# Performance work log

Hardware: AMD Instinct MI355X
Metric: run time of the kernel (lower is better)

Reference implementation:

```python
import jax, jax.numpy as jnp
import numpy as np

B, T, C, H = 128, 256, 64, 128  # batch, seq_len, num_channels, hidden_size


def setup_inputs() -> dict:
    key = jax.random.key(0)
    ks = jax.random.split(key, 7)
    s = 1.0 / np.sqrt(H)  # PyTorch LSTM/Linear init bound
    x = jax.random.normal(ks[0], (B, T, C), dtype=jnp.float32)
    # Per-channel LSTM weights (input_size=1). Gate order i,f,g,o like PyTorch.
    w_ih = jax.random.uniform(ks[1], (C, 4 * H), jnp.float32, -s, s)      # [C,4H] (input is scalar)
    w_hh = jax.random.uniform(ks[2], (C, 4 * H, H), jnp.float32, -s, s)   # [C,4H,H]
    b_ih = jax.random.uniform(ks[3], (C, 4 * H), jnp.float32, -s, s)
    b_hh = jax.random.uniform(ks[4], (C, 4 * H), jnp.float32, -s, s)
    # Per-channel Linear(H, 1) head.
    w_fc = jax.random.uniform(ks[5], (C, H), jnp.float32, -s, s)
    b_fc = jax.random.uniform(ks[6], (C,), jnp.float32, -s, s)
    return {"x": x, "w_ih": w_ih, "w_hh": w_hh, "b_ih": b_ih,
            "b_hh": b_hh, "w_fc": w_fc, "b_fc": b_fc}


def reference(x, w_ih, w_hh, b_ih, b_hh, w_fc, b_fc):
    # x: [B,T,C]. All C channel-LSTMs run as one batched recurrence over [B,C].
    b = b_ih + b_hh  # [C,4H]
    xt = jnp.transpose(x, (1, 0, 2))  # [T,B,C] for scan over time
    h0 = jnp.zeros((x.shape[0], x.shape[2], w_hh.shape[-1]), x.dtype)  # [B,C,H]
    c0 = h0

    def step(carry, x_t):
        h, c = carry  # [B,C,H]
        # scalar input times per-channel input weights + recurrent GEMM
        gates = x_t[..., None] * w_ih + jnp.einsum('bch,cgh->bcg', h, w_hh) + b  # [B,C,4H]
        i, f, g, o = jnp.split(gates, 4, axis=-1)
        i = jax.nn.sigmoid(i)
        f = jax.nn.sigmoid(f)
        g = jnp.tanh(g)
        o = jax.nn.sigmoid(o)
        c_new = f * c + i * g
        h_new = o * jnp.tanh(c_new)
        return (h_new, c_new), None

    (hT, _), _ = jax.lax.scan(step, (h0, c0), xt)
    # Per-channel linear head on the last hidden state -> [B,C]
    return jnp.einsum('bch,ch->bc', hT, w_fc) + b_fc
```

## Files before the change

kernel.cpp:

```cpp
#include <hip/hip_runtime.h>
#include <hip/hip_bf16.h>

typedef __bf16 bf16_t;
typedef bf16_t bf16x8 __attribute__((ext_vector_type(8)));
typedef float f32x4 __attribute__((ext_vector_type(4)));
typedef float f32x2 __attribute__((ext_vector_type(2)));

#define B_   128
#define T_   256
#define C_   64
#define H_   128
#define G_   512
#define BT   16
#define HBUF 2048

#define K1 1.4426950408889634f
#define K2 2.8853900817779268f

union AF { bf16x8 v; uint32_t w[4]; };

__device__ __forceinline__ uint32_t cvt_pk_bf16(float a, float b) {
    uint32_t r; asm("v_cvt_pk_bf16_f32 %0, %1, %2" : "=v"(r) : "v"(a), "v"(b)); return r;
}
__device__ __forceinline__ f32x2 exp2v(f32x2 z) {
    f32x2 r; r.x = __builtin_amdgcn_exp2f(z.x); r.y = __builtin_amdgcn_exp2f(z.y); return r;
}
__device__ __forceinline__ f32x2 rcpv(f32x2 z) {
    f32x2 r; r.x = __builtin_amdgcn_rcpf(z.x); r.y = __builtin_amdgcn_rcpf(z.y); return r;
}

__global__ __launch_bounds__(512, 4) void lstm_fused(
    const float* __restrict__ x,
    const float* __restrict__ w_ih,
    const float* __restrict__ w_hh,
    const float* __restrict__ b_ih,
    const float* __restrict__ b_hh,
    const float* __restrict__ w_fc,
    const float* __restrict__ b_fc,
    float* __restrict__ out)
{
    const int c    = blockIdx.x & (C_ - 1);
    const int bt   = blockIdx.x >> 6;
    const int b0   = bt * BT;
    const int tid  = threadIdx.x;
    const int w    = tid >> 6;
    const int lane = tid & 63;
    const int l16  = lane & 15;
    const int lg   = lane >> 4;
    const bool lg0 = (lg == 0);

    __shared__ __align__(16) bf16_t h_lds[2 * HBUF];
    __shared__ __align__(16) float x_lds[T_ * BT];

    for (int i = tid; i < HBUF; i += 512) ((uint32_t*)h_lds)[i] = 0u;
    for (int i = tid; i < BT * T_; i += 512) {
        const int bl = i >> 8, t = i & 255;
        x_lds[t * BT + bl] = x[(size_t)(b0 + bl) * (T_ * C_) + (size_t)t * C_ + c];
    }

    bf16x8 bw[4][4];
    AF     augb[4];
    #pragma unroll
    for (int q = 0; q < 4; ++q) {
        const float s = (q == 2) ? K2 : -K1;
        const int n = q * 128 + w * 16 + l16;
        #pragma unroll
        for (int kk = 0; kk < 4; ++kk) {
            const int k0 = kk * 32 + lg * 8;
            const float4 wa = *(const float4*)&w_hh[((size_t)(c * G_ + n)) * H_ + k0];
            const float4 wb = *(const float4*)&w_hh[((size_t)(c * G_ + n)) * H_ + k0 + 4];
            bf16x8 g;
            g[0] = (bf16_t)(s * wa.x); g[1] = (bf16_t)(s * wa.y);
            g[2] = (bf16_t)(s * wa.z); g[3] = (bf16_t)(s * wa.w);
            g[4] = (bf16_t)(s * wb.x); g[5] = (bf16_t)(s * wb.y);
            g[6] = (bf16_t)(s * wb.z); g[7] = (bf16_t)(s * wb.w);
            bw[q][kk] = g;
        }
        const float wv = s * w_ih[c * G_ + n];
        const bf16_t wh = (bf16_t)wv;
        const bf16_t wl = (bf16_t)(wv - (float)wh);
        const float bb = s * (b_ih[c * G_ + n] + b_hh[c * G_ + n]);
        const bf16_t bh = (bf16_t)bb;
        const bf16_t bl2 = (bf16_t)(bb - (float)bh);
        bf16x8 f;
        #pragma unroll
        for (int e = 0; e < 8; ++e) f[e] = (bf16_t)0.0f;
        if (lg0) { f[0] = wh; f[1] = wl; f[2] = wh; f[3] = bh; f[4] = bl2; }
        augb[q].v = f;
    }

    float cst[4] = {0.f, 0.f, 0.f, 0.f};
    const f32x4 zc = {0.f, 0.f, 0.f, 0.f};
    const f32x2 one2 = {1.f, 1.f};

    __syncthreads();

    const int a_off = l16 * 8;
    const int wbase = (w * 2 + (l16 >> 3)) * 128 + lg * 32 + (l16 & 7);

    auto step = [&](const int RD, const int WR, const int t) {
        const float xr = x_lds[t * BT + l16];
        const uint32_t p0 = cvt_pk_bf16(xr, xr);
        const float xhf = __uint_as_float(p0 << 16);
        const uint32_t p1 = cvt_pk_bf16(xr - xhf, 1.0f);
        AF a4;
        a4.w[0] = lg0 ? p0 : 0u;
        a4.w[1] = lg0 ? p1 : 0u;
        a4.w[2] = lg0 ? 0x00003F80u : 0u;
        a4.w[3] = 0u;

        f32x4 acc[4];
        {
            #pragma unroll
            for (int q = 0; q < 4; ++q)
                acc[q] = __builtin_amdgcn_mfma_f32_16x16x32_bf16(a4.v, augb[q].v, zc, 0, 0, 0);
        }
        #pragma unroll
        for (int kk = 0; kk < 4; ++kk) {
            const bf16x8 a = *(const bf16x8*)&h_lds[RD + (kk * 4 + lg) * 128 + a_off];
            #pragma unroll
            for (int q = 0; q < 4; ++q)
                acc[q] = __builtin_amdgcn_mfma_f32_16x16x32_bf16(a, bw[q][kk], acc[q], 0, 0, 0);
        }

        #pragma unroll
        for (int p = 0; p < 2; ++p) {
            f32x2 zi = {acc[0][2*p], acc[0][2*p+1]};
            f32x2 zf = {acc[1][2*p], acc[1][2*p+1]};
            f32x2 zg = {acc[2][2*p], acc[2][2*p+1]};
            f32x2 zo = {acc[3][2*p], acc[3][2*p+1]};
            const f32x2 ei = exp2v(zi), ef = exp2v(zf), eg = exp2v(zg), eo = exp2v(zo);
            const f32x2 A2 = one2 + ei, D2 = one2 + ef, B2 = one2 + eg, O2 = one2 + eo;
            const f32x2 AB = A2 * B2;
            const f32x2 r1 = rcpv(D2 * AB);
            f32x2 cs = {cst[2*p], cst[2*p+1]};
            const f32x2 cn = (D2 * (eg - one2) + cs * AB) * r1;
            cst[2*p] = cn.x; cst[2*p+1] = cn.y;
            f32x2 m2 = K2 * cn;
            m2 = __builtin_elementwise_min(__builtin_elementwise_max(m2, f32x2{-60.f,-60.f}), f32x2{60.f,60.f});
            const f32x2 ec = exp2v(m2);
            const f32x2 r2 = rcpv(O2 * (one2 + ec));
            const f32x2 hv = (ec - one2) * r2;
            h_lds[WR + wbase + (2*p)   * 8] = (bf16_t)hv.x;
            h_lds[WR + wbase + (2*p+1) * 8] = (bf16_t)hv.y;
        }
        __syncthreads();
    };

    for (int t = 0; t < T_; t += 2) {
        step(0, HBUF, t);
        step(HBUF, 0, t + 1);
    }

    #pragma unroll
    for (int rr = 0; rr < 2; ++rr) {
        const int row = w * 2 + rr;
        const int eaddr = (lane >> 2) * 128 + row * 8 + (lane & 3) * 2;
        const float h0 = (float)h_lds[eaddr];
        const float h1 = (float)h_lds[eaddr + 1];
        const float2 wf = *(const float2*)&w_fc[c * H_ + 2 * lane];
        float p = h0 * wf.x + h1 * wf.y;
        #pragma unroll
        for (int off = 32; off; off >>= 1) p += __shfl_xor(p, off);
        if (lane == 0) out[(size_t)(b0 + row) * C_ + c] = p + b_fc[c];
    }
}

extern "C" void kernel_launch(void* const* d_in, const int* in_sizes, int n_in,
                              void* d_out, int out_size, void* d_ws, size_t ws_size,
                              hipStream_t stream) {
    const float* x    = (const float*)d_in[0];
    const float* w_ih = (const float*)d_in[1];
    const float* w_hh = (const float*)d_in[2];
    const float* b_ih = (const float*)d_in[3];
    const float* b_hh = (const float*)d_in[4];
    const float* w_fc = (const float*)d_in[5];
    const float* b_fc = (const float*)d_in[6];
    float* out = (float*)d_out;

    dim3 grid(C_ * (B_ / BT));
    dim3 block(512);
    lstm_fused<<<grid, block, 0, stream>>>(x, w_ih, w_hh, b_ih, b_hh, w_fc, b_fc, out);
}
```

Baseline: 347.5 us.

## Interleave two channels per block to overlap MFMA with gate activations

Each block now processes two channels, and the loop staggers them so one channel's recurrent MFMAs run while the other channel's gate activations are computed. The aim is to hide the serial latency of the MFMA→activation→sync chain. The input and bias term moves from an augmented MFMA to fp32 FMAs. Reciprocals are shared between pairs and the tanh clamp uses fmed3. The grid halves, occupancy bounds drop to 2 blocks per CU, and per-thread register pressure doubles, so fewer blocks fill the GPU.

```diff
diff --git a/kernel.cpp b/kernel.cpp
--- a/kernel.cpp
+++ b/kernel.cpp
@@ -12,24 +12,19 @@
 #define H_   128
 #define G_   512
 #define BT   16
-#define HBUF 2048
 
 #define K1 1.4426950408889634f
 #define K2 2.8853900817779268f
 
-union AF { bf16x8 v; uint32_t w[4]; };
-
-__device__ __forceinline__ uint32_t cvt_pk_bf16(float a, float b) {
-    uint32_t r; asm("v_cvt_pk_bf16_f32 %0, %1, %2" : "=v"(r) : "v"(a), "v"(b)); return r;
-}
 __device__ __forceinline__ f32x2 exp2v(f32x2 z) {
     f32x2 r; r.x = __builtin_amdgcn_exp2f(z.x); r.y = __builtin_amdgcn_exp2f(z.y); return r;
 }
-__device__ __forceinline__ f32x2 rcpv(f32x2 z) {
-    f32x2 r; r.x = __builtin_amdgcn_rcpf(z.x); r.y = __builtin_amdgcn_rcpf(z.y); return r;
+__device__ __forceinline__ f32x2 rcp_pair(f32x2 d) {
+    const float q = __builtin_amdgcn_rcpf(d.x * d.y);
+    f32x2 r; r.x = q * d.y; r.y = q * d.x; return r;
 }
 
-__global__ __launch_bounds__(512, 4) void lstm_fused(
+__global__ __launch_bounds__(512, 2) void lstm_fused(
     const float* __restrict__ x,
     const float* __restrict__ w_ih,
     const float* __restrict__ w_hh,
@@ -39,130 +34,125 @@
     const float* __restrict__ b_fc,
     float* __restrict__ out)
 {
-    const int c    = blockIdx.x & (C_ - 1);
-    const int bt   = blockIdx.x >> 6;
+    const int cp   = blockIdx.x & 31;
+    const int bt   = blockIdx.x >> 5;
+    const int c0   = cp * 2;
     const int b0   = bt * BT;
     const int tid  = threadIdx.x;
     const int w    = tid >> 6;
     const int lane = tid & 63;
     const int l16  = lane & 15;
     const int lg   = lane >> 4;
-    const bool lg0 = (lg == 0);
 
-    __shared__ __align__(16) bf16_t h_lds[2 * HBUF];
-    __shared__ __align__(16) float x_lds[T_ * BT];
+    __shared__ __align__(16) bf16_t h_lds[2][2048];
+    __shared__ __align__(16) float  x_lds[2][T_ * BT];
 
-    for (int i = tid; i < HBUF; i += 512) ((uint32_t*)h_lds)[i] = 0u;
-    for (int i = tid; i < BT * T_; i += 512) {
-        const int bl = i >> 8, t = i & 255;
-        x_lds[t * BT + bl] = x[(size_t)(b0 + bl) * (T_ * C_) + (size_t)t * C_ + c];
+    for (int i = tid; i < 2048; i += 512) ((uint32_t*)h_lds)[i] = 0u;
+    for (int i = tid; i < 2 * BT * T_; i += 512) {
+        const int j = i >> 12, idx = i & 4095;
+        const int bl = idx >> 8, t = idx & 255;
+        x_lds[j][t * BT + bl] = x[(size_t)(b0 + bl) * (T_ * C_) + (size_t)t * C_ + c0 + j];
     }
 
-    bf16x8 bw[4][4];
-    AF     augb[4];
+    bf16x8 bw[2][4][4];
+    float  wih[2][4], bias[2][4];
     #pragma unroll
-    for (int q = 0; q < 4; ++q) {
-        const float s = (q == 2) ? K2 : -K1;
-        const int n = q * 128 + w * 16 + l16;
+    for (int j = 0; j < 2; ++j) {
+        const int c = c0 + j;
+        #pragma unroll
+        for (int q = 0; q < 4; ++q) {
+            const float s = (q == 2) ? K2 : -K1;
+            const int n = q * 128 + w * 16 + l16;
+            wih[j][q]  = s * w_ih[c * G_ + n];
+            bias[j][q] = s * (b_ih[c * G_ + n] + b_hh[c * G_ + n]);
+            #pragma unroll
+            for (int kk = 0; kk < 4; ++kk) {
+                const int k0 = kk * 32 + lg * 8;
+                const float4 wa = *(const float4*)&w_hh[((size_t)(c * G_ + n)) * H_ + k0];
+                const float4 wb = *(const float4*)&w_hh[((size_t)(c * G_ + n)) * H_ + k0 + 4];
+                bf16x8 g;
+                g[0] = (bf16_t)(s * wa.x); g[1] = (bf16_t)(s * wa.y);
+                g[2] = (bf16_t)(s * wa.z); g[3] = (bf16_t)(s * wa.w);
+                g[4] = (bf16_t)(s * wb.x); g[5] = (bf16_t)(s * wb.y);
+                g[6] = (bf16_t)(s * wb.z); g[7] = (bf16_t)(s * wb.w);
+                bw[j][q][kk] = g;
+            }
+        }
+    }
+
+    f32x4 acc[2][4];
+    float cst[2][4] = {{0.f,0.f,0.f,0.f},{0.f,0.f,0.f,0.f}};
+    const f32x2 one2 = {1.f, 1.f};
+
+    const int a_off = l16 * 8;
+    const int wb_   = (w * 2 + (l16 >> 3)) * 128 + lg * 32 + (l16 & 7);
+
+    auto MF = [&](const int j, const int t) {
+        const f32x4 xv = *(const f32x4*)&x_lds[j][t * BT + lg * 4];
+        #pragma unroll
+        for (int q = 0; q < 4; ++q)
+            #pragma unroll
+            for (int r = 0; r < 4; ++r)
+                acc[j][q][r] = fmaf(xv[r], wih[j][q], bias[j][q]);
         #pragma unroll
         for (int kk = 0; kk < 4; ++kk) {
-            const int k0 = kk * 32 + lg * 8;
-            const float4 wa = *(const float4*)&w_hh[((size_t)(c * G_ + n)) * H_ + k0];
-            const float4 wb = *(const float4*)&w_hh[((size_t)(c * G_ + n)) * H_ + k0 + 4];
-            bf16x8 g;
-            g[0] = (bf16_t)(s * wa.x); g[1] = (bf16_t)(s * wa.y);
-            g[2] = (bf16_t)(s * wa.z); g[3] = (bf16_t)(s * wa.w);
-            g[4] = (bf16_t)(s * wb.x); g[5] = (bf16_t)(s * wb.y);
-            g[6] = (bf16_t)(s * wb.z); g[7] = (bf16_t)(s * wb.w);
-            bw[q][kk] = g;
+            const bf16x8 a = *(const bf16x8*)&h_lds[j][(kk * 4 + lg) * 128 + a_off];
+            #pragma unroll
+            for (int q = 0; q < 4; ++q)
+                acc[j][q] = __builtin_amdgcn_mfma_f32_16x16x32_bf16(a, bw[j][q][kk], acc[j][q], 0, 0, 0);
         }
-        const float wv = s * w_ih[c * G_ + n];
-        const bf16_t wh = (bf16_t)wv;
-        const bf16_t wl = (bf16_t)(wv - (float)wh);
-        const float bb = s * (b_ih[c * G_ + n] + b_hh[c * G_ + n]);
-        const bf16_t bh = (bf16_t)bb;
-        const bf16_t bl2 = (bf16_t)(bb - (float)bh);
-        bf16x8 f;
+    };
+
+    auto ACT = [&](const int j) {
         #pragma unroll
-        for (int e = 0; e < 8; ++e) f[e] = (bf16_t)0.0f;
-        if (lg0) { f[0] = wh; f[1] = wl; f[2] = wh; f[3] = bh; f[4] = bl2; }
-        augb[q].v = f;
+        for (int p = 0; p < 2; ++p) {
+            const f32x2 ei = exp2v(f32x2{acc[j][0][2*p], acc[j][0][2*p+1]});
+            const f32x2 ef = exp2v(f32x2{acc[j][1][2*p], acc[j][1][2*p+1]});
+            const f32x2 eg = exp2v(f32x2{acc[j][2][2*p], acc[j][2][2*p+1]});
+            const f32x2 eo = exp2v(f32x2{acc[j][3][2*p], acc[j][3][2*p+1]});
+            const f32x2 A2 = one2 + ei, D2 = one2 + ef, B2 = one2 + eg, O2 = one2 + eo;
+            const f32x2 AB = A2 * B2;
+            const f32x2 r1 = rcp_pair(D2 * AB);
+            const f32x2 cs = {cst[j][2*p], cst[j][2*p+1]};
+            const f32x2 cn = (D2 * (eg - one2) + cs * AB) * r1;
+            cst[j][2*p] = cn.x; cst[j][2*p+1] = cn.y;
+            f32x2 m2;
+            m2.x = __builtin_amdgcn_fmed3f(K2 * cn.x, -24.f, 24.f);
+            m2.y = __builtin_amdgcn_fmed3f(K2 * cn.y, -24.f, 24.f);
+            const f32x2 ec = exp2v(m2);
+            const f32x2 r2 = rcp_pair(O2 * (one2 + ec));
+            const f32x2 hv = (ec - one2) * r2;
+            h_lds[j][wb_ + (2*p)   * 8] = (bf16_t)hv.x;
+            h_lds[j][wb_ + (2*p+1) * 8] = (bf16_t)hv.y;
+        }
+    };
+
+    for (int t = 0; t < T_; ++t) {
+        __syncthreads();
+        MF(0, t);
+        if (t) ACT(1);
+        __syncthreads();
+        MF(1, t);
+        ACT(0);
     }
-
-    float cst[4] = {0.f, 0.f, 0.f, 0.f};
-    const f32x4 zc = {0.f, 0.f, 0.f, 0.f};
-    const f32x2 one2 = {1.f, 1.f};
-
+    ACT(1);
     __syncthreads();
 
-    const int a_off = l16 * 8;
-    const int wbase = (w * 2 + (l16 >> 3)) * 128 + lg * 32 + (l16 & 7);
-
-    auto step = [&](const int RD, const int WR, const int t) {
-        const float xr = x_lds[t * BT + l16];
-        const uint32_t p0 = cvt_pk_bf16(xr, xr);
-        const float xhf = __uint_as_float(p0 << 16);
-        const uint32_t p1 = cvt_pk_bf16(xr - xhf, 1.0f);
-        AF a4;
-        a4.w[0] = lg0 ? p0 : 0u;
-        a4.w[1] = lg0 ? p1 : 0u;
-        a4.w[2] = lg0 ? 0x00003F80u : 0u;
-        a4.w[3] = 0u;
-
-        f32x4 acc[4];
-        {
+    #pragma unroll
+    for (int j = 0; j < 2; ++j) {
+        const int c = c0 + j;
+        #pragma unroll
+        for (int rr = 0; rr < 2; ++rr) {
+            const int row = w * 2 + rr;
+            const int eaddr = (lane >> 2) * 128 + row * 8 + (lane & 3) * 2;
+            const float h0 = (float)h_lds[j][eaddr];
+            const float h1 = (float)h_lds[j][eaddr + 1];
+            const float2 wf = *(const float2*)&w_fc[c * H_ + 2 * lane];
+            float p = h0 * wf.x + h1 * wf.y;
             #pragma unroll
-            for (int q = 0; q < 4; ++q)
-                acc[q] = __builtin_amdgcn_mfma_f32_16x16x32_bf16(a4.v, augb[q].v, zc, 0, 0, 0);
+            for (int off = 32; off; off >>= 1) p += __shfl_xor(p, off);
+            if (lane == 0) out[(size_t)(b0 + row) * C_ + c] = p + b_fc[c];
         }
-        #pragma unroll
-        for (int kk = 0; kk < 4; ++kk) {
-            const bf16x8 a = *(const bf16x8*)&h_lds[RD + (kk * 4 + lg) * 128 + a_off];
-            #pragma unroll
-            for (int q = 0; q < 4; ++q)
-                acc[q] = __builtin_amdgcn_mfma_f32_16x16x32_bf16(a, bw[q][kk], acc[q], 0, 0, 0);
-        }
-
-        #pragma unroll
-        for (int p = 0; p < 2; ++p) {
-            f32x2 zi = {acc[0][2*p], acc[0][2*p+1]};
-            f32x2 zf = {acc[1][2*p], acc[1][2*p+1]};
-            f32x2 zg = {acc[2][2*p], acc[2][2*p+1]};
-            f32x2 zo = {acc[3][2*p], acc[3][2*p+1]};
-            const f32x2 ei = exp2v(zi), ef = exp2v(zf), eg = exp2v(zg), eo = exp2v(zo);
-            const f32x2 A2 = one2 + ei, D2 = one2 + ef, B2 = one2 + eg, O2 = one2 + eo;
-            const f32x2 AB = A2 * B2;
-            const f32x2 r1 = rcpv(D2 * AB);
-            f32x2 cs = {cst[2*p], cst[2*p+1]};
-            const f32x2 cn = (D2 * (eg - one2) + cs * AB) * r1;
-            cst[2*p] = cn.x; cst[2*p+1] = cn.y;
-            f32x2 m2 = K2 * cn;
-            m2 = __builtin_elementwise_min(__builtin_elementwise_max(m2, f32x2{-60.f,-60.f}), f32x2{60.f,60.f});
-            const f32x2 ec = exp2v(m2);
-            const f32x2 r2 = rcpv(O2 * (one2 + ec));
-            const f32x2 hv = (ec - one2) * r2;
-            h_lds[WR + wbase + (2*p)   * 8] = (bf16_t)hv.x;
-            h_lds[WR + wbase + (2*p+1) * 8] = (bf16_t)hv.y;
-        }
-        __syncthreads();
-    };
-
-    for (int t = 0; t < T_; t += 2) {
-        step(0, HBUF, t);
-        step(HBUF, 0, t + 1);
-    }
-
-    #pragma unroll
-    for (int rr = 0; rr < 2; ++rr) {
-        const int row = w * 2 + rr;
-        const int eaddr = (lane >> 2) * 128 + row * 8 + (lane & 3) * 2;
-        const float h0 = (float)h_lds[eaddr];
-        const float h1 = (float)h_lds[eaddr + 1];
-        const float2 wf = *(const float2*)&w_fc[c * H_ + 2 * lane];
-        float p = h0 * wf.x + h1 * wf.y;
-        #pragma unroll
-        for (int off = 32; off; off >>= 1) p += __shfl_xor(p, off);
-        if (lane == 0) out[(size_t)(b0 + row) * C_ + c] = p + b_fc[c];
     }
 }
 
@@ -178,7 +168,7 @@
     const float* b_fc = (const float*)d_in[6];
     float* out = (float*)d_out;
 
-    dim3 grid(C_ * (B_ / BT));
+    dim3 grid((C_ / 2) * (B_ / BT));
     dim3 block(512);
     lstm_fused<<<grid, block, 0, stream>>>(x, w_ih, w_hh, b_ih, b_hh, w_fc, b_fc, out);
 }
```

After: 407.2 us. 1.17x slower.

## Process two batch subtiles per block, interleaving MFMA of one with activations of other

Applied to the files above, without the earlier changes.

Doubles the batch tile per block to two 16-row subtiles, which halves the grid. Each step now issues the recurrent MFMAs for one subtile while the gate activations of the other subtile run, so matrix and transcendental work can overlap within a block. Each subtile keeps a single h buffer, and barriers are placed between the two phases. It also shares one reciprocal across each pair of values and replaces the min/max clamp with fmed3 at a tighter range. The costs are a lower launch-bounds occupancy target, more live accumulator registers, and a higher overflow risk in the paired reciprocal product.

```diff
diff --git a/kernel.cpp b/kernel.cpp
--- a/kernel.cpp
+++ b/kernel.cpp
@@ -11,8 +11,7 @@
 #define C_   64
 #define H_   128
 #define G_   512
-#define BT   16
-#define HBUF 2048
+#define BT   32
 
 #define K1 1.4426950408889634f
 #define K2 2.8853900817779268f
@@ -25,11 +24,12 @@
 __device__ __forceinline__ f32x2 exp2v(f32x2 z) {
     f32x2 r; r.x = __builtin_amdgcn_exp2f(z.x); r.y = __builtin_amdgcn_exp2f(z.y); return r;
 }
-__device__ __forceinline__ f32x2 rcpv(f32x2 z) {
-    f32x2 r; r.x = __builtin_amdgcn_rcpf(z.x); r.y = __builtin_amdgcn_rcpf(z.y); return r;
+__device__ __forceinline__ f32x2 rcp_pair(f32x2 d) {
+    const float q = __builtin_amdgcn_rcpf(d.x * d.y);
+    f32x2 r; r.x = q * d.y; r.y = q * d.x; return r;
 }
 
-__global__ __launch_bounds__(512, 4) void lstm_fused(
+__global__ __launch_bounds__(512, 2) void lstm_fused(
     const float* __restrict__ x,
     const float* __restrict__ w_ih,
     const float* __restrict__ w_hh,
@@ -49,13 +49,13 @@
     const int lg   = lane >> 4;
     const bool lg0 = (lg == 0);
 
-    __shared__ __align__(16) bf16_t h_lds[2 * HBUF];
-    __shared__ __align__(16) float x_lds[T_ * BT];
+    __shared__ __align__(16) bf16_t h_lds[2][2048];
+    __shared__ __align__(16) float  x_lds[T_ * BT];
 
-    for (int i = tid; i < HBUF; i += 512) ((uint32_t*)h_lds)[i] = 0u;
+    for (int i = tid; i < 2048; i += 512) ((uint32_t*)h_lds)[i] = 0u;
     for (int i = tid; i < BT * T_; i += 512) {
-        const int bl = i >> 8, t = i & 255;
-        x_lds[t * BT + bl] = x[(size_t)(b0 + bl) * (T_ * C_) + (size_t)t * C_ + c];
+        const int row = i >> 8, t = i & 255;
+        x_lds[t * BT + row] = x[(size_t)(b0 + row) * (T_ * C_) + (size_t)t * C_ + c];
     }
 
     bf16x8 bw[4][4];
@@ -80,7 +80,7 @@
         const bf16_t wh = (bf16_t)wv;
         const bf16_t wl = (bf16_t)(wv - (float)wh);
         const float bb = s * (b_ih[c * G_ + n] + b_hh[c * G_ + n]);
-        const bf16_t bh = (bf16_t)bb;
+        const bf16_t bh  = (bf16_t)bb;
         const bf16_t bl2 = (bf16_t)(bb - (float)bh);
         bf16x8 f;
         #pragma unroll
@@ -89,17 +89,16 @@
         augb[q].v = f;
     }
 
-    float cst[4] = {0.f, 0.f, 0.f, 0.f};
+    f32x4 acc[2][4];
+    float cst[2][4] = {{0.f,0.f,0.f,0.f},{0.f,0.f,0.f,0.f}};
     const f32x4 zc = {0.f, 0.f, 0.f, 0.f};
     const f32x2 one2 = {1.f, 1.f};
 
-    __syncthreads();
+    const int a_off = l16 * 8;
+    const int wb_   = (w * 2 + (l16 >> 3)) * 128 + lg * 32 + (l16 & 7);
 
-    const int a_off = l16 * 8;
-    const int wbase = (w * 2 + (l16 >> 3)) * 128 + lg * 32 + (l16 & 7);
-
-    auto step = [&](const int RD, const int WR, const int t) {
-        const float xr = x_lds[t * BT + l16];
+    auto MF = [&](const int s, const int t) {
+        const float xr = x_lds[t * BT + s * 16 + l16];
         const uint32_t p0 = cvt_pk_bf16(xr, xr);
         const float xhf = __uint_as_float(p0 << 16);
         const uint32_t p1 = cvt_pk_bf16(xr - xhf, 1.0f);
@@ -108,56 +107,66 @@
         a4.w[1] = lg0 ? p1 : 0u;
         a4.w[2] = lg0 ? 0x00003F80u : 0u;
         a4.w[3] = 0u;
-
-        f32x4 acc[4];
-        {
+        #pragma unroll
+        for (int q = 0; q < 4; ++q)
+            acc[s][q] = __builtin_amdgcn_mfma_f32_16x16x32_bf16(a4.v, augb[q].v, zc, 0, 0, 0);
+        #pragma unroll
+        for (int kk = 0; kk < 4; ++kk) {
+            const bf16x8 a = *(const bf16x8*)&h_lds[s][(kk * 4 + lg) * 128 + a_off];
             #pragma unroll
             for (int q = 0; q < 4; ++q)
-                acc[q] = __builtin_amdgcn_mfma_f32_16x16x32_bf16(a4.v, augb[q].v, zc, 0, 0, 0);
+                acc[s][q] = __builtin_amdgcn_mfma_f32_16x16x32_bf16(a, bw[q][kk], acc[s][q], 0, 0, 0);
         }
-        #pragma unroll
-        for (int kk = 0; kk < 4; ++kk) {
-            const bf16x8 a = *(const bf16x8*)&h_lds[RD + (kk * 4 + lg) * 128 + a_off];
-            #pragma unroll
-            for (int q = 0; q < 4; ++q)
-                acc[q] = __builtin_amdgcn_mfma_f32_16x16x32_bf16(a, bw[q][kk], acc[q], 0, 0, 0);
-        }
+    };
 
+    auto ACT = [&](const int s) {
         #pragma unroll
         for (int p = 0; p < 2; ++p) {
-            f32x2 zi = {acc[0][2*p], acc[0][2*p+1]};
-            f32x2 zf = {acc[1][2*p], acc[1][2*p+1]};
-            f32x2 zg = {acc[2][2*p], acc[2][2*p+1]};
-            f32x2 zo = {acc[3][2*p], acc[3][2*p+1]};
-            const f32x2 ei = exp2v(zi), ef = exp2v(zf), eg = exp2v(zg), eo = exp2v(zo);
+            const f32x2 ei = exp2v(f32x2{acc[s][0][2*p], acc[s][0][2*p+1]});
+            const f32x2 ef = exp2v(f32x2{acc[s][1][2*p], acc[s][1][2*p+1]});
+            const f32x2 eg = exp2v(f32x2{acc[s][2][2*p], acc[s][2][2*p+1]});
+            const f32x2 eo = exp2v(f32x2{acc[s][3][2*p], acc[s][3][2*p+1]});
             const f32x2 A2 = one2 + ei, D2 = one2 + ef, B2 = one2 + eg, O2 = one2 + eo;
             const f32x2 AB = A2 * B2;
-            const f32x2 r1 = rcpv(D2 * AB);
-            f32x2 cs = {cst[2*p], cst[2*p+1]};
+            const f32x2 r1 = rcp_pair(D2 * AB);
+            const f32x2 cs = {cst[s][2*p], cst[s][2*p+1]};
             const f32x2 cn = (D2 * (eg - one2) + cs * AB) * r1;
-            cst[2*p] = cn.x; cst[2*p+1] = cn.y;
-            f32x2 m2 = K2 * cn;
-            m2 = __builtin_elementwise_min(__builtin_elementwise_max(m2, f32x2{-60.f,-60.f}), f32x2{60.f,60.f});
+            cst[s][2*p] = cn.x; cst[s][2*p+1] = cn.y;
+            f32x2 m2;
+            m2.x = __builtin_amdgcn_fmed3f(K2 * cn.x, -24.f, 24.f);
+            m2.y = __builtin_amdgcn_fmed3f(K2 * cn.y, -24.f, 24.f);
             const f32x2 ec = exp2v(m2);
-            const f32x2 r2 = rcpv(O2 * (one2 + ec));
+            const f32x2 r2 = rcp_pair(O2 * (one2 + ec));
             const f32x2 hv = (ec - one2) * r2;
-            h_lds[WR + wbase + (2*p)   * 8] = (bf16_t)hv.x;
-            h_lds[WR + wbase + (2*p+1) * 8] = (bf16_t)hv.y;
+            h_lds[s][wb_ + (2*p)   * 8] = (bf16_t)hv.x;
+            h_lds[s][wb_ + (2*p+1) * 8] = (bf16_t)hv.y;
         }
-        __syncthreads();
     };
 
-    for (int t = 0; t < T_; t += 2) {
-        step(0, HBUF, t);
-        step(HBUF, 0, t + 1);
+    __syncthreads();
+    MF(0, 0);
+    __syncthreads();
+    MF(1, 0);
+    ACT(0);
+    for (int t = 1; t < T_; ++t) {
+        __syncthreads();
+        MF(0, t);
+        ACT(1);
+        __syncthreads();
+        MF(1, t);
+        ACT(0);
     }
+    ACT(1);
+    __syncthreads();
 
     #pragma unroll
-    for (int rr = 0; rr < 2; ++rr) {
-        const int row = w * 2 + rr;
-        const int eaddr = (lane >> 2) * 128 + row * 8 + (lane & 3) * 2;
-        const float h0 = (float)h_lds[eaddr];
-        const float h1 = (float)h_lds[eaddr + 1];
+    for (int rr = 0; rr < 4; ++rr) {
+        const int row = w * 4 + rr;
+        const int s   = row >> 4;
+        const int lr  = row & 15;
+        const int eaddr = (lane >> 2) * 128 + lr * 8 + (lane & 3) * 2;
+        const float h0 = (float)h_lds[s][eaddr];
+        const float h1 = (float)h_lds[s][eaddr + 1];
         const float2 wf = *(const float2*)&w_fc[c * H_ + 2 * lane];
         float p = h0 * wf.x + h1 * wf.y;
         #pragma unroll
```

New measurement: 407.2 us. +17.2%, slower.
